# Kernel tuning notes

Hardware: AMD Instinct MI355X
Metric: run time of the kernel (lower is better)

The kernel has to match this reference:

```python
import jax, jax.numpy as jnp
import numpy as np

N = 100000
E = 6400000
H = 64  # hidden_nf


def setup_inputs() -> dict:
    key = jax.random.key(0)
    ks = jax.random.split(key, 12)
    x = jax.random.normal(ks[0], (N, 3), dtype=jnp.float32)
    vel = jax.random.normal(ks[1], (N, 3), dtype=jnp.float32)
    vel_norm = jax.random.uniform(ks[2], (N, 1), dtype=jnp.float32)
    edge_index = jax.random.randint(ks[3], (2, E), 0, N, dtype=jnp.int32)
    # coord_mlp_vel: Linear(1,H) -> LeakyReLU(0.2) -> Linear(H,1)
    W1 = jax.random.normal(ks[4], (H, 1), dtype=jnp.float32) * (1.0 / np.sqrt(1))
    b1 = jnp.zeros((H,), dtype=jnp.float32)
    W2 = jax.random.normal(ks[5], (1, H), dtype=jnp.float32) * (1.0 / np.sqrt(H))
    b2 = jnp.zeros((1,), dtype=jnp.float32)
    # phi: Linear(1,H) -> LeakyReLU(0.2) -> Linear(H,1,bias=False, xavier gain=0.001) -> Tanh
    Wp1 = jax.random.normal(ks[6], (H, 1), dtype=jnp.float32) * (1.0 / np.sqrt(1))
    bp1 = jnp.zeros((H,), dtype=jnp.float32)
    Wp2 = jax.random.normal(ks[7], (1, H), dtype=jnp.float32) * 0.001
    return {"x": x, "vel_norm": vel_norm, "vel": vel, "edge_index": edge_index,
            "W1": W1, "b1": b1, "W2": W2, "b2": b2,
            "Wp1": Wp1, "bp1": bp1, "Wp2": Wp2}


def reference(x, vel_norm, vel, edge_index, W1, b1, W2, b2, Wp1, bp1, Wp2):
    row, col = edge_index[0], edge_index[1]
    # edge_model: gather endpoint positions, radial distance -> tiny MLP -> scaled diff
    x_diff = x[row] - x[col]                                   # [E, 3]
    radial = jnp.sqrt(jnp.sum(x_diff * x_diff, axis=1, keepdims=True))  # [E, 1]
    h = jax.nn.leaky_relu(radial @ Wp1.T + bp1, 0.2)           # [E, H]
    e_out = jnp.tanh(h @ Wp2.T)                                # [E, 1]
    m_ij = x_diff * e_out                                      # [E, 3]
    # node_model: unsorted_segment_mean over row
    agg_sum = jax.ops.segment_sum(m_ij, row, num_segments=x.shape[0])           # [N, 3]
    cnt = jax.ops.segment_sum(jnp.ones((m_ij.shape[0], 1), m_ij.dtype), row,
                              num_segments=x.shape[0])                           # [N, 1]
    x_out = x + agg_sum / jnp.maximum(cnt, 1.0)
    # velocity term: x + vel * coord_mlp_vel(vel_norm)
    hv = jax.nn.leaky_relu(vel_norm @ W1.T + b1, 0.2)          # [N, H]
    scale = hv @ W2.T + b2                                     # [N, 1]
    return x_out + vel * scale
```

## Files before the change

kernel.cpp:

```cpp
#include <hip/hip_runtime.h>
#include <hip/hip_fp16.h>
#include <math.h>

#define LEAKY 0.2f
#define HDIM 64
#define EPB 4096
#define TPB1 256
#define PERT (EPB / TPB1)
#define RANGE 1024
#define RSH 10
#define KMAX 128
#define NSUB 4
#define NSLICE 8
#define FS2 262144.0f
#define INVFS2 (1.0f / 262144.0f)
#define FBIAS 4194304


__device__ __forceinline__ float fast_tanh(float v) {
    float e = __builtin_amdgcn_exp2f(v * 2.88539008178f);
    return 1.0f - 2.0f * __builtin_amdgcn_rcpf(e + 1.0f);
}

__device__ __forceinline__ float edge_eo(float rad, float C, bool slow,
                                         const float* sW1, const float* sb1,
                                         const float* sW2) {
    if (!slow) return fast_tanh(C * rad);
    float a = 0.f;
    #pragma unroll
    for (int k = 0; k < HDIM; k++) {
        float h = fmaf(rad, sW1[k], sb1[k]);
        h = (h > 0.f) ? h : LEAKY * h;
        a = fmaf(sW2[k], h, a);
    }
    return fast_tanh(a);
}

__global__ void repack_h_kernel(const float* __restrict__ x, uint2* __restrict__ xh, int N,
                                const float* __restrict__ Wp1, const float* __restrict__ bp1,
                                const float* __restrict__ Wp2, float* __restrict__ consts,
                                uint4* __restrict__ acc4, unsigned* __restrict__ cursor, int K) {
    int i = blockIdx.x * blockDim.x + threadIdx.x;
    if (i < N) {
        unsigned hx = __half_as_ushort(__float2half(x[3*i]));
        unsigned hy = __half_as_ushort(__float2half(x[3*i+1]));
        unsigned hz = __half_as_ushort(__float2half(x[3*i+2]));
        xh[i] = make_uint2((hy << 16) | hx, hz);
        acc4[i] = make_uint4(0u, 0u, 0u, 0u);
    }
    if (blockIdx.x == 0) {
        if (threadIdx.x < 64) {
            int k = threadIdx.x;
            float w1 = Wp1[k];
            float slope = (w1 >= 0.f) ? 1.f : LEAKY;
            float c = Wp2[k] * w1 * slope;
            float bnz = (bp1[k] != 0.f) ? 1.f : 0.f;
            #pragma unroll
            for (int off = 32; off > 0; off >>= 1) {
                c += __shfl_down(c, off, 64);
                bnz += __shfl_down(bnz, off, 64);
            }
            if (k == 0) { consts[0] = c; consts[1] = bnz; }
        }
        for (int k = threadIdx.x; k < NSUB * K; k += 256) cursor[k] = 0u;
    }
}

__device__ void overflow_edge(unsigned rec, unsigned b_, const uint2* __restrict__ xh,
                              float C, bool slow,
                              const float* __restrict__ Wp1, const float* __restrict__ bp1,
                              const float* __restrict__ Wp2, unsigned* __restrict__ acc4) {
    unsigned lid = rec >> 17, col = rec & 0x1FFFFu;
    unsigned row = b_ * RANGE + lid;
    uint2 ga = xh[row], gb = xh[col];
    float ax = __half2float(__ushort_as_half((unsigned short)(ga.x & 0xFFFF)));
    float ay = __half2float(__ushort_as_half((unsigned short)(ga.x >> 16)));
    float az = __half2float(__ushort_as_half((unsigned short)(ga.y & 0xFFFF)));
    float bx = __half2float(__ushort_as_half((unsigned short)(gb.x & 0xFFFF)));
    float by = __half2float(__ushort_as_half((unsigned short)(gb.x >> 16)));
    float bz = __half2float(__ushort_as_half((unsigned short)(gb.y & 0xFFFF)));
    float dx = ax - bx, dy = ay - by, dz = az - bz;
    float rad = sqrtf(dx*dx + dy*dy + dz*dz);
    float eo;
    if (!slow) {
        eo = fast_tanh(C * rad);
    } else {
        float a = 0.f;
        for (int k = 0; k < HDIM; k++) {
            float h = fmaf(rad, Wp1[k], bp1[k]);
            h = (h > 0.f) ? h : LEAKY * h;
            a = fmaf(Wp2[k], h, a);
        }
        eo = fast_tanh(a);
    }
    atomicAdd(&acc4[4*row + 0], (unsigned)__float2int_rn(dx * eo * FS2));
    atomicAdd(&acc4[4*row + 1], (unsigned)__float2int_rn(dy * eo * FS2));
    atomicAdd(&acc4[4*row + 2], (unsigned)__float2int_rn(dz * eo * FS2));
    atomicAdd(&acc4[4*row + 3], 1u);
}

__global__ __launch_bounds__(TPB1) void sort4_kernel(
        const int* __restrict__ ei,
        const uint2* __restrict__ xh,
        const float* __restrict__ Wp1, const float* __restrict__ bp1,
        const float* __restrict__ Wp2, const float* __restrict__ consts,
        unsigned* __restrict__ cursor, unsigned* __restrict__ acc4,
        unsigned* __restrict__ recs, int E, int K, unsigned csub) {
    __shared__ unsigned stage[EPB];
    __shared__ unsigned char bucket_of[EPB];
    __shared__ unsigned hist[KMAX];
    __shared__ unsigned scanv[KMAX + 1];
    __shared__ unsigned cur[KMAX];
    __shared__ unsigned gstart[KMAX];
    const float C = consts[0];
    const bool slow = (consts[1] != 0.f);
    const unsigned sub = (unsigned)blockIdx.x & (NSUB - 1);
    for (int k = threadIdx.x; k < K; k += TPB1) hist[k] = 0;
    __syncthreads();

    const size_t base = (size_t)blockIdx.x * EPB;
    const unsigned t = threadIdx.x;
    unsigned rc[PERT];
    unsigned bk[PERT];
    if (base + EPB <= (size_t)E && (E & 3) == 0) {
        const int4* pr = (const int4*)(ei + base);
        const int4* pc = (const int4*)(ei + (size_t)E + base);
        #pragma unroll
        for (int q = 0; q < PERT / 4; q++) {
            int4 rv = pr[t + q * TPB1];
            int4 cv = pc[t + q * TPB1];
            rc[4*q+0] = (((unsigned)rv.x & (RANGE-1)) << 17) | (unsigned)cv.x;
            rc[4*q+1] = (((unsigned)rv.y & (RANGE-1)) << 17) | (unsigned)cv.y;
            rc[4*q+2] = (((unsigned)rv.z & (RANGE-1)) << 17) | (unsigned)cv.z;
            rc[4*q+3] = (((unsigned)rv.w & (RANGE-1)) << 17) | (unsigned)cv.w;
            bk[4*q+0] = (unsigned)rv.x >> RSH;
            bk[4*q+1] = (unsigned)rv.y >> RSH;
            bk[4*q+2] = (unsigned)rv.z >> RSH;
            bk[4*q+3] = (unsigned)rv.w >> RSH;
        }
        #pragma unroll
        for (int i = 0; i < PERT; i++) atomicAdd(&hist[bk[i]], 1u);
    } else {
        #pragma unroll
        for (int i = 0; i < PERT; i++) {
            size_t e = base + (size_t)i * TPB1 + t;
            bk[i] = 0xFFFFFFFFu;
            if (e < (size_t)E) {
                unsigned r = (unsigned)ei[e];
                unsigned c = (unsigned)ei[(size_t)E + e];
                rc[i] = ((r & (RANGE-1)) << 17) | c;
                bk[i] = r >> RSH;
                atomicAdd(&hist[bk[i]], 1u);
            }
        }
    }
    __syncthreads();
    unsigned res = 0;
    if (t < (unsigned)K) {
        unsigned myc = hist[t];
        if (myc) res = atomicAdd(&cursor[t * NSUB + sub], myc);
    }
    if (t >= 192) {
        int l = t - 192;
        unsigned origA = (l < K) ? hist[l] : 0u;
        unsigned origB = (l + 64 < K) ? hist[l + 64] : 0u;
        unsigned a = origA, b = origB;
        #pragma unroll
        for (int off = 1; off < 64; off <<= 1) {
            unsigned va = __shfl_up(a, off, 64);
            unsigned vb = __shfl_up(b, off, 64);
            if (l >= off) { a += va; b += vb; }
        }
        unsigned totA = __shfl(a, 63, 64);
        unsigned grand = totA + __shfl(b, 63, 64);
        unsigned exA = a - origA;
        unsigned exB = totA + b - origB;
        scanv[l] = exA;  cur[l] = exA;
        scanv[l + 64] = exB;  cur[l + 64] = exB;
        if (l == 63) scanv[K] = grand;
    }
    __syncthreads();
    #pragma unroll
    for (int i = 0; i < PERT; i++) {
        if (bk[i] != 0xFFFFFFFFu) {
            unsigned slot = atomicAdd(&cur[bk[i]], 1u);
            stage[slot] = rc[i];
            bucket_of[slot] = (unsigned char)bk[i];
        }
    }
    if (t < (unsigned)K) gstart[t] = res;
    __syncthreads();
    unsigned total = scanv[K];
    for (unsigned j = t; j < total; j += TPB1) {
        unsigned b_ = bucket_of[j];
        unsigned off = gstart[b_] + (j - scanv[b_]);
        if (off < csub) recs[(size_t)(b_ * NSUB + sub) * csub + off] = stage[j];
        else            overflow_edge(stage[j], b_, xh, C, slow, Wp1, bp1, Wp2, acc4);
    }
}

__global__ __launch_bounds__(256) void reduce6_kernel(
        const unsigned* __restrict__ recs, const unsigned* __restrict__ cursor,
        const uint2* __restrict__ xh,
        const float* __restrict__ Wp1, const float* __restrict__ bp1,
        const float* __restrict__ Wp2, const float* __restrict__ consts,
        uint4* __restrict__ slices, int N, int K, unsigned csub) {
    __shared__ unsigned long long accA[RANGE];
    __shared__ unsigned long long accB[RANGE];
    __shared__ float sW1[HDIM], sb1[HDIM], sW2[HDIM];
    const int b = blockIdx.x / NSLICE;
    const int s = blockIdx.x % NSLICE;
    const int r = s & (NSUB - 1);
    const int p = s / NSUB;
    const float C = consts[0];
    const bool slow = (consts[1] != 0.f);
    if (slow) {
        for (int k = threadIdx.x; k < HDIM; k += 256) {
            sW1[k] = Wp1[k]; sb1[k] = bp1[k]; sW2[k] = Wp2[k];
        }
    }
    for (int i = threadIdx.x; i < RANGE; i += 256) { accA[i] = 0ull; accB[i] = 0ull; }
    __syncthreads();
    const int nbase = b * RANGE;
    unsigned cnt = cursor[b * NSUB + r];
    if (cnt > csub) cnt = csub;
    unsigned quads = (cnt + 3) >> 2;
    unsigned perq = (quads + 1) >> 1;
    unsigned q0 = (unsigned)p * perq;
    unsigned q1 = q0 + perq; if (q1 > quads) q1 = quads;
    const uint4* rb4 = (const uint4*)(recs + (size_t)(b * NSUB + r) * csub);
    for (unsigned q = q0 + threadIdx.x; q < q1; q += 256) {
        uint4 v = rb4[q];
        unsigned idx = 4 * q;
        unsigned rv[4] = {v.x, v.y, v.z, v.w};
        #pragma unroll
        for (int u = 0; u < 4; u++) {
            if (idx + u < cnt) {
                unsigned rec = rv[u];
                unsigned lid = rec >> 17, col = rec & 0x1FFFFu;
                uint2 ga = xh[nbase + lid];
                uint2 gb = xh[col];
                float ax = __half2float(__ushort_as_half((unsigned short)(ga.x & 0xFFFF)));
                float ay = __half2float(__ushort_as_half((unsigned short)(ga.x >> 16)));
                float az = __half2float(__ushort_as_half((unsigned short)(ga.y & 0xFFFF)));
                float bx = __half2float(__ushort_as_half((unsigned short)(gb.x & 0xFFFF)));
                float by = __half2float(__ushort_as_half((unsigned short)(gb.x >> 16)));
                float bz = __half2float(__ushort_as_half((unsigned short)(gb.y & 0xFFFF)));
                float dx = ax - bx, dy = ay - by, dz = az - bz;
                float rad = sqrtf(dx*dx + dy*dy + dz*dz);
                float eo = edge_eo(rad, C, slow, sW1, sb1, sW2);
                unsigned ix = (unsigned)(__float2int_rn(dx * eo * FS2) + FBIAS);
                unsigned iy = (unsigned)(__float2int_rn(dy * eo * FS2) + FBIAS);
                unsigned iz = (unsigned)(__float2int_rn(dz * eo * FS2) + FBIAS);
                atomicAdd(&accA[lid], ((unsigned long long)ix << 32) | (unsigned long long)iy);
                atomicAdd(&accB[lid], ((unsigned long long)iz << 32) | 1ull);
            }
        }
    }
    __syncthreads();
    for (int i = threadIdx.x; i < RANGE; i += 256) {
        int node = nbase + i;
        if (node < N) {
            unsigned long long A = accA[i], B = accB[i];
            slices[(size_t)s * N + node] =
                make_uint4((unsigned)(A >> 32), (unsigned)A,
                           (unsigned)(B >> 32), (unsigned)B);
        }
    }
}

__global__ void node_merge_kernel(const float* __restrict__ x,
                                  const float* __restrict__ vel_norm,
                                  const float* __restrict__ vel,
                                  const float* __restrict__ W1, const float* __restrict__ b1,
                                  const float* __restrict__ W2, const float* __restrict__ b2,
                                  const uint4* __restrict__ slices,
                                  const uint4* __restrict__ acc4,
                                  float* __restrict__ out, int N) {
    __shared__ float sW1[HDIM], sb1[HDIM], sW2[HDIM];
    for (int k = threadIdx.x; k < HDIM; k += blockDim.x) {
        sW1[k] = W1[k]; sb1[k] = b1[k]; sW2[k] = W2[k];
    }
    __syncthreads();
    int i = blockIdx.x * blockDim.x + threadIdx.x;
    if (i >= N) return;
    unsigned long long sxb = 0, syb = 0, szb = 0;
    unsigned sc = 0;
    #pragma unroll
    for (int s = 0; s < NSLICE; s++) {
        uint4 v = slices[(size_t)s * N + i];
        sxb += v.x; syb += v.y; szb += v.z; sc += v.w;
    }
    uint4 a4 = acc4[i];
    long long fx = (long long)sxb - (long long)sc * (long long)FBIAS + (long long)(int)a4.x;
    long long fy = (long long)syb - (long long)sc * (long long)FBIAS + (long long)(int)a4.y;
    long long fz = (long long)szb - (long long)sc * (long long)FBIAS + (long long)(int)a4.z;
    float cntf = (float)(sc + a4.w);
    float sx = (float)fx * INVFS2;
    float sy = (float)fy * INVFS2;
    float sz = (float)fz * INVFS2;
    float vn = vel_norm[i];
    float a = b2[0];
    #pragma unroll
    for (int k = 0; k < HDIM; k++) {
        float h = fmaf(vn, sW1[k], sb1[k]);
        h = (h > 0.f) ? h : LEAKY * h;
        a = fmaf(sW2[k], h, a);
    }
    float inv = 1.0f / fmaxf(cntf, 1.0f);
    out[3*i]     = x[3*i]     + sx * inv + vel[3*i]     * a;
    out[3*i + 1] = x[3*i + 1] + sy * inv + vel[3*i + 1] * a;
    out[3*i + 2] = x[3*i + 2] + sz * inv + vel[3*i + 2] * a;
}

__global__ void precompute_kernel(const float* __restrict__ Wp1,
                                  const float* __restrict__ bp1,
                                  const float* __restrict__ Wp2,
                                  float* __restrict__ consts) {
    int k = threadIdx.x;
    float w1 = Wp1[k];
    float slope = (w1 >= 0.f) ? 1.f : LEAKY;
    float c = Wp2[k] * w1 * slope;
    float bnz = (bp1[k] != 0.f) ? 1.f : 0.f;
    #pragma unroll
    for (int off = 32; off > 0; off >>= 1) {
        c += __shfl_down(c, off, 64);
        bnz += __shfl_down(bnz, off, 64);
    }
    if (k == 0) { consts[0] = c; consts[1] = bnz; }
}

__global__ void edge_atomic_kernel(const float* __restrict__ x, const int* __restrict__ ei,
                                   const float* __restrict__ Wp1, const float* __restrict__ bp1,
                                   const float* __restrict__ Wp2, const float* __restrict__ consts,
                                   float* __restrict__ acc, int E) {
    __shared__ float sW1[HDIM], sb1[HDIM], sW2[HDIM];
    const float C = consts[0];
    const bool slow = (consts[1] != 0.f);
    if (slow) {
        for (int k = threadIdx.x; k < HDIM; k += blockDim.x) {
            sW1[k] = Wp1[k]; sb1[k] = bp1[k]; sW2[k] = Wp2[k];
        }
        __syncthreads();
    }
    int e = blockIdx.x * blockDim.x + threadIdx.x;
    if (e >= E) return;
    int r = ei[e];
    int c = ei[E + e];
    float dx = x[3*r] - x[3*c];
    float dy = x[3*r+1] - x[3*c+1];
    float dz = x[3*r+2] - x[3*c+2];
    float rad = sqrtf(dx*dx + dy*dy + dz*dz);
    float eo = edge_eo(rad, C, slow, sW1, sb1, sW2);
    float* basep = acc + ((size_t)r << 2);
    atomicAdd(basep + 0, dx * eo);
    atomicAdd(basep + 1, dy * eo);
    atomicAdd(basep + 2, dz * eo);
    atomicAdd(basep + 3, 1.f);
}

__global__ void node_kernel(const float* __restrict__ x, const float* __restrict__ vel_norm,
                            const float* __restrict__ vel,
                            const float* __restrict__ W1, const float* __restrict__ b1,
                            const float* __restrict__ W2, const float* __restrict__ b2,
                            const float4* __restrict__ slices,
                            float* __restrict__ out, int N, int S) {
    __shared__ float sW1[HDIM], sb1[HDIM], sW2[HDIM];
    for (int k = threadIdx.x; k < HDIM; k += blockDim.x) {
        sW1[k] = W1[k]; sb1[k] = b1[k]; sW2[k] = W2[k];
    }
    __syncthreads();
    int i = blockIdx.x * blockDim.x + threadIdx.x;
    if (i >= N) return;
    float sx = 0.f, sy = 0.f, sz = 0.f, sc = 0.f;
    for (int s = 0; s < S; s++) {
        float4 v = slices[(size_t)s * N + i];
        sx += v.x; sy += v.y; sz += v.z; sc += v.w;
    }
    float vn = vel_norm[i];
    float a = b2[0];
    #pragma unroll
    for (int k = 0; k < HDIM; k++) {
        float h = fmaf(vn, sW1[k], sb1[k]);
        h = (h > 0.f) ? h : LEAKY * h;
        a = fmaf(sW2[k], h, a);
    }
    float inv = 1.0f / fmaxf(sc, 1.0f);
    out[3*i]     = x[3*i]     + sx * inv + vel[3*i]     * a;
    out[3*i + 1] = x[3*i + 1] + sy * inv + vel[3*i + 1] * a;
    out[3*i + 2] = x[3*i + 2] + sz * inv + vel[3*i + 2] * a;
}

extern "C" void kernel_launch(void* const* d_in, const int* in_sizes, int n_in,
                              void* d_out, int out_size, void* d_ws, size_t ws_size,
                              hipStream_t stream) {
    const float* x        = (const float*)d_in[0];
    const float* vel_norm = (const float*)d_in[1];
    const float* vel      = (const float*)d_in[2];
    const int*   ei       = (const int*)  d_in[3];
    const float* W1       = (const float*)d_in[4];
    const float* b1       = (const float*)d_in[5];
    const float* W2       = (const float*)d_in[6];
    const float* b2       = (const float*)d_in[7];
    const float* Wp1      = (const float*)d_in[8];
    const float* bp1      = (const float*)d_in[9];
    const float* Wp2      = (const float*)d_in[10];

    const int N = in_sizes[0] / 3;
    const int E = in_sizes[3] / 2;
    const int K = (N + RANGE - 1) / RANGE;
    const int nblk = (E + EPB - 1) / EPB;

    unsigned csub = (unsigned)(E / (K * NSUB)) + 1024u;
    csub = (csub + 63u) & ~63u;

    size_t rec_bytes = (size_t)K * NSUB * csub * sizeof(unsigned);
    size_t sp_slices = (rec_bytes + 15) & ~(size_t)15;
    size_t sp_xh     = sp_slices + (size_t)NSLICE * N * sizeof(uint4);
    size_t sp_acc    = (sp_xh + (size_t)N * sizeof(uint2) + 15) & ~(size_t)15;
    size_t sp_cur    = sp_acc + (size_t)N * sizeof(uint4);
    size_t sp_const  = (sp_cur + (size_t)NSUB * KMAX * sizeof(unsigned) + 15) & ~(size_t)15;
    size_t need      = sp_const + 32;

    if (K <= KMAX && ws_size >= need) {
        unsigned* recs   = (unsigned*)d_ws;
        uint4*    slices = (uint4*)   ((char*)d_ws + sp_slices);
        uint2*    xh     = (uint2*)   ((char*)d_ws + sp_xh);
        unsigned* acc4   = (unsigned*)((char*)d_ws + sp_acc);
        unsigned* cursor = (unsigned*)((char*)d_ws + sp_cur);
        float*    consts = (float*)   ((char*)d_ws + sp_const);

        repack_h_kernel<<<(N + 255) / 256, 256, 0, stream>>>(
            x, xh, N, Wp1, bp1, Wp2, consts, (uint4*)acc4, cursor, K);
        sort4_kernel<<<nblk, TPB1, 0, stream>>>(
            ei, xh, Wp1, bp1, Wp2, consts, cursor, acc4, recs, E, K, csub);
        reduce6_kernel<<<K * NSLICE, 256, 0, stream>>>(
            recs, cursor, xh, Wp1, bp1, Wp2, consts, slices, N, K, csub);
        node_merge_kernel<<<(N + 255) / 256, 256, 0, stream>>>(
            x, vel_norm, vel, W1, b1, W2, b2, slices, (const uint4*)acc4,
            (float*)d_out, N);
    } else {
        float* acc    = (float*)d_ws;
        float* consts = (float*)((char*)d_ws + (size_t)N * sizeof(float4));
        hipMemsetAsync(d_ws, 0, (size_t)N * sizeof(float4) + 32, stream);
        precompute_kernel<<<1, 64, 0, stream>>>(Wp1, bp1, Wp2, consts);
        edge_atomic_kernel<<<(E + 255) / 256, 256, 0, stream>>>(x, ei, Wp1, bp1, Wp2,
                                                                consts, acc, E);
        node_kernel<<<(N + 255) / 256, 256, 0, stream>>>(x, vel_norm, vel, W1, b1, W2, b2,
                                                         (const float4*)acc, (float*)d_out, N, 1);
    }
}
```

Before: 208.2 us.

## Double reduce slices, cache row positions in LDS, and unroll record loop

The reduce kernel now splits each bucket's records across 16 slices instead of 8, which gives more blocks and more parallelism. Each block first copies its 1024 row-node positions into shared memory, so row lookups hit LDS instead of global memory. The record loop is unrolled two-deep for more memory-level parallelism, and the slow MLP path is moved into a noinline function to reduce register pressure, with launch bounds requesting 4 blocks per SM. In exchange, node_merge must read twice as many slice partials, which adds merge traffic.

```diff
diff --git a/kernel.cpp b/kernel.cpp
--- a/kernel.cpp
+++ b/kernel.cpp
@@ -11,7 +11,7 @@
 #define RSH 10
 #define KMAX 128
 #define NSUB 4
-#define NSLICE 8
+#define NSLICE 16
 #define FS2 262144.0f
 #define INVFS2 (1.0f / 262144.0f)
 #define FBIAS 4194304
@@ -22,12 +22,11 @@
     return 1.0f - 2.0f * __builtin_amdgcn_rcpf(e + 1.0f);
 }
 
-__device__ __forceinline__ float edge_eo(float rad, float C, bool slow,
-                                         const float* sW1, const float* sb1,
-                                         const float* sW2) {
-    if (!slow) return fast_tanh(C * rad);
+__device__ __noinline__ float edge_eo_slow(float rad,
+                                           const float* sW1, const float* sb1,
+                                           const float* sW2) {
     float a = 0.f;
-    #pragma unroll
+    #pragma unroll 1
     for (int k = 0; k < HDIM; k++) {
         float h = fmaf(rad, sW1[k], sb1[k]);
         h = (h > 0.f) ? h : LEAKY * h;
@@ -66,7 +65,7 @@
     }
 }
 
-__device__ void overflow_edge(unsigned rec, unsigned b_, const uint2* __restrict__ xh,
+__device__ __noinline__ void overflow_edge(unsigned rec, unsigned b_, const uint2* __restrict__ xh,
                               float C, bool slow,
                               const float* __restrict__ Wp1, const float* __restrict__ bp1,
                               const float* __restrict__ Wp2, unsigned* __restrict__ acc4) {
@@ -199,7 +198,7 @@
     }
 }
 
-__global__ __launch_bounds__(256) void reduce6_kernel(
+__global__ __launch_bounds__(256, 4) void reduce7_kernel(
         const unsigned* __restrict__ recs, const unsigned* __restrict__ cursor,
         const uint2* __restrict__ xh,
         const float* __restrict__ Wp1, const float* __restrict__ bp1,
@@ -207,56 +206,75 @@
         uint4* __restrict__ slices, int N, int K, unsigned csub) {
     __shared__ unsigned long long accA[RANGE];
     __shared__ unsigned long long accB[RANGE];
+    __shared__ uint2 sxh[RANGE];
     __shared__ float sW1[HDIM], sb1[HDIM], sW2[HDIM];
     const int b = blockIdx.x / NSLICE;
     const int s = blockIdx.x % NSLICE;
     const int r = s & (NSUB - 1);
-    const int p = s / NSUB;
+    const int p = s >> 2;
     const float C = consts[0];
     const bool slow = (consts[1] != 0.f);
+    const int nbase = b * RANGE;
     if (slow) {
         for (int k = threadIdx.x; k < HDIM; k += 256) {
             sW1[k] = Wp1[k]; sb1[k] = bp1[k]; sW2[k] = Wp2[k];
         }
     }
-    for (int i = threadIdx.x; i < RANGE; i += 256) { accA[i] = 0ull; accB[i] = 0ull; }
-    __syncthreads();
-    const int nbase = b * RANGE;
+    for (int i = threadIdx.x; i < RANGE; i += 256) {
+        accA[i] = 0ull; accB[i] = 0ull;
+        int src = nbase + i;
+        sxh[i] = xh[(src < N) ? src : 0];
+    }
+    __syncthreads();
     unsigned cnt = cursor[b * NSUB + r];
     if (cnt > csub) cnt = csub;
     unsigned quads = (cnt + 3) >> 2;
-    unsigned perq = (quads + 1) >> 1;
+    unsigned perq = (quads + 3) >> 2;
     unsigned q0 = (unsigned)p * perq;
     unsigned q1 = q0 + perq; if (q1 > quads) q1 = quads;
     const uint4* rb4 = (const uint4*)(recs + (size_t)(b * NSUB + r) * csub);
-    for (unsigned q = q0 + threadIdx.x; q < q1; q += 256) {
+
+    #define PROC_REC(rec, idx)                                                     \
+        if ((idx) < cnt) {                                                         \
+            unsigned lid_ = (rec) >> 17, col_ = (rec) & 0x1FFFFu;                  \
+            uint2 ga = sxh[lid_];                                                  \
+            uint2 gb = xh[col_];                                                   \
+            float ax = __half2float(__ushort_as_half((unsigned short)(ga.x & 0xFFFF))); \
+            float ay = __half2float(__ushort_as_half((unsigned short)(ga.x >> 16)));    \
+            float az = __half2float(__ushort_as_half((unsigned short)(ga.y & 0xFFFF))); \
+            float bx = __half2float(__ushort_as_half((unsigned short)(gb.x & 0xFFFF))); \
+            float by = __half2float(__ushort_as_half((unsigned short)(gb.x >> 16)));    \
+            float bz = __half2float(__ushort_as_half((unsigned short)(gb.y & 0xFFFF))); \
+            float dx = ax - bx, dy = ay - by, dz = az - bz;                        \
+            float rad = sqrtf(dx*dx + dy*dy + dz*dz);                              \
+            float eo = slow ? edge_eo_slow(rad, sW1, sb1, sW2)                     \
+                            : fast_tanh(C * rad);                                  \
+            unsigned ix = (unsigned)(__float2int_rn(dx * eo * FS2) + FBIAS);       \
+            unsigned iy = (unsigned)(__float2int_rn(dy * eo * FS2) + FBIAS);       \
+            unsigned iz = (unsigned)(__float2int_rn(dz * eo * FS2) + FBIAS);       \
+            atomicAdd(&accA[lid_], ((unsigned long long)ix << 32) | (unsigned long long)iy); \
+            atomicAdd(&accB[lid_], ((unsigned long long)iz << 32) | 1ull);         \
+        }
+
+    unsigned q = q0 + threadIdx.x;
+    while (q + 256 < q1) {
+        uint4 v0 = rb4[q];
+        uint4 v1 = rb4[q + 256];
+        unsigned i0 = 4 * q, i1 = 4 * (q + 256);
+        PROC_REC(v0.x, i0); PROC_REC(v0.y, i0 + 1);
+        PROC_REC(v0.z, i0 + 2); PROC_REC(v0.w, i0 + 3);
+        PROC_REC(v1.x, i1); PROC_REC(v1.y, i1 + 1);
+        PROC_REC(v1.z, i1 + 2); PROC_REC(v1.w, i1 + 3);
+        q += 512;
+    }
+    while (q < q1) {
         uint4 v = rb4[q];
-        unsigned idx = 4 * q;
-        unsigned rv[4] = {v.x, v.y, v.z, v.w};
-        #pragma unroll
-        for (int u = 0; u < 4; u++) {
-            if (idx + u < cnt) {
-                unsigned rec = rv[u];
-                unsigned lid = rec >> 17, col = rec & 0x1FFFFu;
-                uint2 ga = xh[nbase + lid];
-                uint2 gb = xh[col];
-                float ax = __half2float(__ushort_as_half((unsigned short)(ga.x & 0xFFFF)));
-                float ay = __half2float(__ushort_as_half((unsigned short)(ga.x >> 16)));
-                float az = __half2float(__ushort_as_half((unsigned short)(ga.y & 0xFFFF)));
-                float bx = __half2float(__ushort_as_half((unsigned short)(gb.x & 0xFFFF)));
-                float by = __half2float(__ushort_as_half((unsigned short)(gb.x >> 16)));
-                float bz = __half2float(__ushort_as_half((unsigned short)(gb.y & 0xFFFF)));
-                float dx = ax - bx, dy = ay - by, dz = az - bz;
-                float rad = sqrtf(dx*dx + dy*dy + dz*dz);
-                float eo = edge_eo(rad, C, slow, sW1, sb1, sW2);
-                unsigned ix = (unsigned)(__float2int_rn(dx * eo * FS2) + FBIAS);
-                unsigned iy = (unsigned)(__float2int_rn(dy * eo * FS2) + FBIAS);
-                unsigned iz = (unsigned)(__float2int_rn(dz * eo * FS2) + FBIAS);
-                atomicAdd(&accA[lid], ((unsigned long long)ix << 32) | (unsigned long long)iy);
-                atomicAdd(&accB[lid], ((unsigned long long)iz << 32) | 1ull);
-            }
-        }
-    }
+        unsigned i0 = 4 * q;
+        PROC_REC(v.x, i0); PROC_REC(v.y, i0 + 1);
+        PROC_REC(v.z, i0 + 2); PROC_REC(v.w, i0 + 3);
+        q += 256;
+    }
+    #undef PROC_REC
     __syncthreads();
     for (int i = threadIdx.x; i < RANGE; i += 256) {
         int node = nbase + i;
@@ -351,7 +369,18 @@
     float dy = x[3*r+1] - x[3*c+1];
     float dz = x[3*r+2] - x[3*c+2];
     float rad = sqrtf(dx*dx + dy*dy + dz*dz);
-    float eo = edge_eo(rad, C, slow, sW1, sb1, sW2);
+    float eo;
+    if (!slow) {
+        eo = fast_tanh(C * rad);
+    } else {
+        float a = 0.f;
+        for (int k = 0; k < HDIM; k++) {
+            float h = fmaf(rad, sW1[k], sb1[k]);
+            h = (h > 0.f) ? h : LEAKY * h;
+            a = fmaf(sW2[k], h, a);
+        }
+        eo = fast_tanh(a);
+    }
     float* basep = acc + ((size_t)r << 2);
     atomicAdd(basep + 0, dx * eo);
     atomicAdd(basep + 1, dy * eo);
@@ -434,7 +463,7 @@
             x, xh, N, Wp1, bp1, Wp2, consts, (uint4*)acc4, cursor, K);
         sort4_kernel<<<nblk, TPB1, 0, stream>>>(
             ei, xh, Wp1, bp1, Wp2, consts, cursor, acc4, recs, E, K, csub);
-        reduce6_kernel<<<K * NSLICE, 256, 0, stream>>>(
+        reduce7_kernel<<<K * NSLICE, 256, 0, stream>>>(
             recs, cursor, xh, Wp1, bp1, Wp2, consts, slices, N, K, csub);
         node_merge_kernel<<<(N + 255) / 256, 256, 0, stream>>>(
             x, vel_norm, vel, W1, b1, W2, b2, slices, (const uint4*)acc4,
```

Result: faster. 183.5 us (-11.9%).
